# Kernel tuning notes

Measured on AMD Instinct MI355X. Metric: run time of the kernel, lower is better.

The kernel has to match this reference:

```python
import jax, jax.numpy as jnp
import numpy as np

N_NODES = 100000
N_EDGES = 1600000
N_FEAT = 4
HIDDEN = 128
EMBED = 128
N_GRAPHS = 512


def setup_inputs() -> dict:
    key = jax.random.key(0)
    ks = jax.random.split(key, 12)
    x = jax.random.normal(ks[0], (N_NODES, N_FEAT), dtype=jnp.float32)
    edge_index = jax.random.randint(ks[1], (2, N_EDGES), 0, N_NODES, dtype=jnp.int64)
    batch = jnp.sort(jax.random.randint(ks[2], (N_NODES,), 0, N_GRAPHS, dtype=jnp.int64))
    def glorot(k, fan_in, fan_out):
        s = jnp.sqrt(6.0 / (fan_in + fan_out))
        return jax.random.uniform(k, (fan_in, fan_out), jnp.float32, -s, s)
    return {
        "x": x,
        "edge_index": edge_index,
        "batch": batch,
        "W_d1": glorot(ks[3], N_FEAT, N_FEAT),
        "b_d1": jnp.zeros((N_FEAT,), jnp.float32),
        "W_g1": glorot(ks[4], N_FEAT, HIDDEN),
        "b_g1": jnp.zeros((HIDDEN,), jnp.float32),
        "W_g2": glorot(ks[5], HIDDEN, HIDDEN),
        "b_g2": jnp.zeros((HIDDEN,), jnp.float32),
        "W_g3": glorot(ks[6], HIDDEN, HIDDEN),
        "b_g3": jnp.zeros((HIDDEN,), jnp.float32),
        "W_d2": glorot(ks[7], HIDDEN, EMBED),
        "b_d2": jnp.zeros((EMBED,), jnp.float32),
    }


def _gcn(x, W, b, src, dst, norm, n_nodes):
    # GCNConv: out[dst] += norm_e * (x @ W)[src], plus bias
    h = x @ W                      # [N, Dout]
    msg = h[src] * norm[:, None]   # [E+N, Dout] (self-loops included)
    out = jax.ops.segment_sum(msg, dst, num_segments=n_nodes)
    return out + b


def reference(x, edge_index, batch, W_d1, b_d1, W_g1, b_g1, W_g2, b_g2, W_g3, b_g3, W_d2, b_d2):
    n = x.shape[0]
    # add self-loops (PyG GCNConv default add_self_loops=True)
    loop = jnp.arange(n, dtype=edge_index.dtype)
    src = jnp.concatenate([edge_index[0], loop])
    dst = jnp.concatenate([edge_index[1], loop])
    # symmetric degree normalization: deg computed over target (col)
    deg = jax.ops.segment_sum(jnp.ones_like(dst, dtype=x.dtype), dst, num_segments=n)
    dis = jnp.where(deg > 0, jax.lax.rsqrt(jnp.maximum(deg, 1.0)), 0.0)
    norm = dis[src] * dis[dst]     # [E+N]

    h = jax.nn.relu(x @ W_d1 + b_d1)
    h = jax.nn.relu(_gcn(h, W_g1, b_g1, src, dst, norm, n))
    h = jax.nn.relu(_gcn(h, W_g2, b_g2, src, dst, norm, n))
    h = jax.nn.relu(_gcn(h, W_g3, b_g3, src, dst, norm, n))

    # global_mean_pool over batch assignment
    sums = jax.ops.segment_sum(h, batch, num_segments=N_GRAPHS)
    cnts = jax.ops.segment_sum(jnp.ones((n,), h.dtype), batch, num_segments=N_GRAPHS)
    pooled = sums / jnp.maximum(cnts, 1.0)[:, None]
    # dropout p=0.3 is identity in eval mode
    return pooled @ W_d2 + b_d2
```

## Files before the change

kernel.cpp:

```cpp
#include <hip/hip_runtime.h>
#include <hip/hip_fp16.h>


#define BSHIFT 8
#define BSZ    256
#define MAXBKT 512
#define CPAD   32
#define CAPSH  13

typedef _Float16 half8 __attribute__((ext_vector_type(8)));
typedef float f32x4 __attribute__((ext_vector_type(4)));
typedef float f32x2 __attribute__((ext_vector_type(2)));

#define RFL __builtin_amdgcn_readfirstlane

__global__ __launch_bounds__(512) void k_prep(
        const float* __restrict__ x, const float* __restrict__ Wd1,
        const float* __restrict__ bd1, __half* __restrict__ h0,
        const float* __restrict__ W2, const float* __restrict__ W3,
        __half* __restrict__ WT2, __half* __restrict__ WT3,
        const int* __restrict__ batch, int* __restrict__ gs,
        const int* __restrict__ src, const int* __restrict__ dst,
        int* __restrict__ bktFill, int* __restrict__ staged,
        float* __restrict__ sums,
        int N, int NG, int E, int nbkt, int BINB, int L1B, int NB1) {
    __shared__ int hh[MAXBKT], base[MAXBKT], cur[MAXBKT];
    int bid = blockIdx.x;
    int t = threadIdx.x;
    if (bid < BINB) {
        for (int i = t; i < nbkt; i += 512) { hh[i] = 0; cur[i] = 0; }
        __syncthreads();
        int e0 = bid * 4096 + t;
#pragma unroll
        for (int k = 0; k < 8; k++) {
            int e = e0 + k * 512;
            if (e < E) atomicAdd(&hh[dst[e] >> BSHIFT], 1);
        }
        __syncthreads();
        for (int i = t; i < nbkt; i += 512)
            base[i] = hh[i] ? atomicAdd(&bktFill[(size_t)i * CPAD], hh[i]) : 0;
        __syncthreads();
#pragma unroll
        for (int k = 0; k < 8; k++) {
            int e = e0 + k * 512;
            if (e < E) {
                int d = dst[e], s = src[e];
                int b = d >> BSHIFT;
                int off = atomicAdd(&cur[b], 1);
                staged[((size_t)b << CAPSH) + base[b] + off] =
                    ((d & (BSZ - 1)) << 17) | s;
            }
        }
    } else if (bid < BINB + L1B) {
        int node = (bid - BINB) * 512 + t;
        if (node < N) {
            float4 xv = ((const float4*)x)[node];
            float h[4];
#pragma unroll
            for (int k = 0; k < 4; k++) {
                float v = xv.x * Wd1[k] + xv.y * Wd1[4 + k]
                        + xv.z * Wd1[8 + k] + xv.w * Wd1[12 + k] + bd1[k];
                h[k] = fmaxf(v, 0.f);
            }
            __half2 o01 = __floats2half2_rn(h[0], h[1]);
            __half2 o23 = __floats2half2_rn(h[2], h[3]);
            uint2 pk;
            pk.x = *(unsigned*)&o01; pk.y = *(unsigned*)&o23;
            *(uint2*)(h0 + (size_t)node * 4) = pk;
        }
    } else if (bid < BINB + L1B + 32) {
        int t2 = (bid - BINB - L1B) * 512 + t;
        int k = t2 >> 7, nn = t2 & 127;
        WT2[nn * 128 + k] = __float2half_rn(W2[t2]);
        WT3[nn * 128 + k] = __float2half_rn(W3[t2]);
    } else if (bid < BINB + L1B + 32 + NB1) {
        int i = (bid - BINB - L1B - 32) * 512 + t;
        if (i >= N) return;
        int b = batch[i];
        int prev = (i == 0) ? -1 : batch[i - 1];
        for (int g2 = prev + 1; g2 <= b; ++g2) gs[g2] = i;
        if (i == N - 1)
            for (int g2 = b + 1; g2 <= NG; ++g2) gs[g2] = N;
    } else {
        int idx = (bid - BINB - L1B - 32 - NB1) * 512 + t;
        if (idx < NG * 128) sums[idx] = 0.f;
    }
}

__global__ __launch_bounds__(1024) void k_fineB(
        const int* __restrict__ staged, const int* __restrict__ bktFill,
        int2* __restrict__ rpe, float* __restrict__ dis,
        int* __restrict__ col, const __half* __restrict__ h0,
        __half* __restrict__ h0s, int N) {
    __shared__ int sEnt[1 << CAPSH];
    __shared__ int cnt[BSZ];
    __shared__ int incl[BSZ];
    int b = blockIdx.x;
    int lo = b << CAPSH;
    int cntE = bktFill[(size_t)b * CPAD];
    int n0 = b << BSHIFT;
    int tid = threadIdx.x;
    if (tid < BSZ) cnt[tid] = 0;
    __syncthreads();
    for (int e = tid; e < cntE; e += 1024) {
        int v = staged[lo + e];
        sEnt[e] = v;
        atomicAdd(&cnt[v >> 17], 1);
    }
    __syncthreads();
    int v = 0;
    if (tid < BSZ) { v = cnt[tid]; incl[tid] = v; }
    for (int off = 1; off < BSZ; off <<= 1) {
        __syncthreads();
        int t = (tid < BSZ && tid >= off) ? incl[tid - off] : 0;
        __syncthreads();
        if (tid < BSZ) incl[tid] += t;
    }
    __syncthreads();
    int myofs = 0;
    if (tid < BSZ) {
        myofs = incl[tid] - v;
        int node = n0 + tid;
        if (node < N) {
            rpe[node] = make_int2(lo + myofs, lo + myofs + v);
            float dloc = rsqrtf((float)(v + 1));
            dis[node] = dloc;
            uint2 hv = *(const uint2*)(h0 + (size_t)node * 4);
            float2 a01 = __half22float2(*(__half2*)&hv.x);
            float2 a23 = __half22float2(*(__half2*)&hv.y);
            __half2 o01 = __floats2half2_rn(a01.x * dloc, a01.y * dloc);
            __half2 o23 = __floats2half2_rn(a23.x * dloc, a23.y * dloc);
            uint2 pk;
            pk.x = *(unsigned*)&o01; pk.y = *(unsigned*)&o23;
            *(uint2*)(h0s + (size_t)node * 4) = pk;
        }
    }
    __syncthreads();
    if (tid < BSZ) { incl[tid] = myofs; cnt[tid] = 0; }
    __syncthreads();
    for (int e = tid; e < cntE; e += 1024) {
        int ent = sEnt[e];
        int dl = ent >> 17;
        int pos = lo + incl[dl] + atomicAdd(&cnt[dl], 1);
        col[pos] = ent & 0x1FFFF;
    }
}

__device__ __forceinline__ void addv4(float a[4], uint2 v) {
    float2 x01 = __half22float2(*(__half2*)&v.x);
    float2 x23 = __half22float2(*(__half2*)&v.y);
    a[0] += x01.x; a[1] += x01.y; a[2] += x23.x; a[3] += x23.y;
}

__global__ __launch_bounds__(256) void k_agg4(
        const __half* __restrict__ h0s, const int2* __restrict__ rpe,
        const float* __restrict__ dis, const int* __restrict__ col,
        float4* __restrict__ agg4, int N) {
    int n = blockIdx.x * 256 + threadIdx.x;
    if (n >= N) return;
    int2 re = rpe[n];
    float di = dis[n];
    float a[4];
    {
        uint2 sv = *(const uint2*)(h0s + (size_t)n * 4);
        float2 s01 = __half22float2(*(__half2*)&sv.x);
        float2 s23 = __half22float2(*(__half2*)&sv.y);
        a[0] = s01.x; a[1] = s01.y; a[2] = s23.x; a[3] = s23.y;
    }
    int e = re.x, r1 = re.y;
    for (; e + 3 < r1; e += 4) {
        int c0 = col[e], c1 = col[e + 1], c2 = col[e + 2], c3 = col[e + 3];
        uint2 v0 = *(const uint2*)(h0s + (size_t)c0 * 4);
        uint2 v1 = *(const uint2*)(h0s + (size_t)c1 * 4);
        uint2 v2 = *(const uint2*)(h0s + (size_t)c2 * 4);
        uint2 v3 = *(const uint2*)(h0s + (size_t)c3 * 4);
        addv4(a, v0); addv4(a, v1); addv4(a, v2); addv4(a, v3);
    }
    for (; e < r1; ++e) {
        uint2 v0 = *(const uint2*)(h0s + (size_t)col[e] * 4);
        addv4(a, v0);
    }
    agg4[n] = make_float4(di * a[0], di * a[1], di * a[2], di * a[3]);
}

__device__ __forceinline__ uint2 pack_fp8x8(const float v[8]) {
    int a = 0, b = 0;
    a = __builtin_amdgcn_cvt_pk_fp8_f32(v[0], v[1], a, false);
    a = __builtin_amdgcn_cvt_pk_fp8_f32(v[2], v[3], a, true);
    b = __builtin_amdgcn_cvt_pk_fp8_f32(v[4], v[5], b, false);
    b = __builtin_amdgcn_cvt_pk_fp8_f32(v[6], v[7], b, true);
    return make_uint2((unsigned)a, (unsigned)b);
}

__device__ __forceinline__ void accf8(float acc[4], unsigned u) {
    f32x2 lo = __builtin_amdgcn_cvt_pk_f32_fp8(u, false);
    f32x2 hi = __builtin_amdgcn_cvt_pk_f32_fp8(u, true);
    acc[0] += lo[0]; acc[1] += lo[1]; acc[2] += hi[0]; acc[3] += hi[1];
}

__global__ __launch_bounds__(256) void k_mmL1(
        const float4* __restrict__ agg4, const float* __restrict__ Wg1,
        const float* __restrict__ b1, const __half* __restrict__ WT2,
        const float* __restrict__ dis, unsigned char* __restrict__ qout,
        int n) {
    __shared__ float sW[512];
    __shared__ float sB[128];
    __shared__ _Float16 sH[16 * 136];
    __shared__ _Float16 sO[16 * 136];
    __shared__ float sDis[16];
    int t = threadIdx.x;
    sW[t] = Wg1[t];
    sW[t + 256] = Wg1[t + 256];
    if (t < 128) sB[t] = b1[t];
    int node0 = blockIdx.x * 16;
    int row = t >> 4, seg = t & 15;
    if (t < 16) sDis[t] = (node0 + t < n) ? dis[node0 + t] : 0.f;
    int nodeR = node0 + row;
    float4 av = (nodeR < n) ? agg4[nodeR] : make_float4(0.f, 0.f, 0.f, 0.f);
    __syncthreads();
    half8 hv;
#pragma unroll
    for (int u = 0; u < 8; u++) {
        int j = seg * 8 + u;
        float vv = sB[j] + av.x * sW[j] + av.y * sW[128 + j]
                 + av.z * sW[256 + j] + av.w * sW[384 + j];
        hv[u] = (_Float16)fmaxf(vv, 0.f);
    }
    *(half8*)&sH[row * 136 + seg * 8] = hv;
    __syncthreads();
    int wave = t >> 6, lane = t & 63;
    int q = lane >> 4, c = lane & 15;
    int n0 = wave * 32;
    f32x4 acc0 = {0.f, 0.f, 0.f, 0.f}, acc1 = {0.f, 0.f, 0.f, 0.f};
#pragma unroll
    for (int ks = 0; ks < 4; ks++) {
        int k0 = ks * 32;
        half8 a  = *(half8*)&sH[c * 136 + k0 + q * 8];
        half8 b0 = *(const half8*)(WT2 + (size_t)(n0 + c) * 128 + k0 + q * 8);
        half8 b1v = *(const half8*)(WT2 + (size_t)(n0 + 16 + c) * 128 + k0 + q * 8);
        acc0 = __builtin_amdgcn_mfma_f32_16x16x32_f16(a, b0, acc0, 0, 0, 0);
        acc1 = __builtin_amdgcn_mfma_f32_16x16x32_f16(a, b1v, acc1, 0, 0, 0);
    }
#pragma unroll
    for (int r = 0; r < 4; r++) {
        int rr = q * 4 + r;
        sO[rr * 136 + n0 + c]      = (_Float16)(acc0[r] * sDis[rr]);
        sO[rr * 136 + n0 + 16 + c] = (_Float16)(acc1[r] * sDis[rr]);
    }
    __syncthreads();
    half8 ov = *(half8*)&sO[row * 136 + seg * 8];
    float vv[8];
#pragma unroll
    for (int u = 0; u < 8; u++) vv[u] = (float)ov[u];
    if (nodeR < n)
        *(uint2*)(qout + (size_t)nodeR * 128 + seg * 8) = pack_fp8x8(vv);
}

__device__ __forceinline__ void agg_chunk_f8(
        const unsigned char* __restrict__ g, int colv, int nloc,
        int hf, int sl, float acc[4]) {
    int npair = nloc >> 1;
    int p = 0;
    for (; p + 3 < npair; p += 4) {
        int i2 = p * 2 + hf;
        int s0 = __shfl(colv, i2);
        int s1 = __shfl(colv, i2 + 2);
        int s2 = __shfl(colv, i2 + 4);
        int s3 = __shfl(colv, i2 + 6);
        unsigned u0 = *(const unsigned*)(g + (size_t)s0 * 128 + sl * 4);
        unsigned u1 = *(const unsigned*)(g + (size_t)s1 * 128 + sl * 4);
        unsigned u2 = *(const unsigned*)(g + (size_t)s2 * 128 + sl * 4);
        unsigned u3 = *(const unsigned*)(g + (size_t)s3 * 128 + sl * 4);
        accf8(acc, u0); accf8(acc, u1); accf8(acc, u2); accf8(acc, u3);
    }
    for (; p < npair; ++p) {
        int s0 = __shfl(colv, p * 2 + hf);
        unsigned u0 = *(const unsigned*)(g + (size_t)s0 * 128 + sl * 4);
        accf8(acc, u0);
    }
    if (nloc & 1) {
        int s0 = __shfl(colv, nloc - 1);
        unsigned u0 = *(const unsigned*)(g + (size_t)s0 * 128 + sl * 4);
        if (!hf) accf8(acc, u0);
    }
}

__device__ __forceinline__ void agg_node_f8v(
        const unsigned char* __restrict__ g, const int* __restrict__ col,
        int r0, int r1, int node, int colv, int hf, int sl, int lane,
        float acc[4]) {
    acc[0] = acc[1] = acc[2] = acc[3] = 0.f;
    if (!hf) {
        unsigned su = *(const unsigned*)(g + (size_t)node * 128 + sl * 4);
        accf8(acc, su);
    }
    int deg = r1 - r0;
    int nloc = deg < 64 ? deg : 64;
    agg_chunk_f8(g, colv, nloc, hf, sl, acc);
    for (int base = r0 + 64; base < r1; base += 64) {
        int cv = col[base + lane];
        int nl = r1 - base; if (nl > 64) nl = 64;
        agg_chunk_f8(g, cv, nl, hf, sl, acc);
    }
#pragma unroll
    for (int k = 0; k < 4; k++) acc[k] += __shfl_xor(acc[k], 32);
}

__global__ __launch_bounds__(256) void k_aggmm(
        const unsigned char* __restrict__ qin, const int2* __restrict__ rpe,
        const int* __restrict__ col, const float* __restrict__ dis,
        const float* __restrict__ bias, const __half* __restrict__ WT,
        unsigned char* __restrict__ qout, int n) {
    __shared__ _Float16 sH[16 * 136];
    __shared__ _Float16 sO[16 * 136];
    __shared__ float sDis[16];
    int t = threadIdx.x;
    int wave = t >> 6, lane = t & 63;
    int hf = lane >> 5, sl = lane & 31;
    int node0 = blockIdx.x * 16;
    if (t < 16) sDis[t] = (node0 + t < n) ? dis[node0 + t] : 0.f;
    float4 bb = ((const float4*)bias)[sl];
    int nodeA = node0 + wave * 4;
    int nd0 = RFL(nodeA), nd1 = RFL(nodeA + 1);
    int nd2 = RFL(nodeA + 2), nd3 = RFL(nodeA + 3);
    int r00 = 0, r10 = 0, r01 = 0, r11 = 0;
    int r02 = 0, r12 = 0, r03 = 0, r13 = 0;
    if (nd0 < n) { int2 re = rpe[nd0]; r00 = RFL(re.x); r10 = RFL(re.y); }
    if (nd1 < n) { int2 re = rpe[nd1]; r01 = RFL(re.x); r11 = RFL(re.y); }
    if (nd2 < n) { int2 re = rpe[nd2]; r02 = RFL(re.x); r12 = RFL(re.y); }
    if (nd3 < n) { int2 re = rpe[nd3]; r03 = RFL(re.x); r13 = RFL(re.y); }
    int cv0 = col[r00 + lane];
    int cv1 = col[r01 + lane];
    int cv2 = col[r02 + lane];
    int cv3 = col[r03 + lane];
    float acc[4];
#define AGGMM_NODE(I, ND, R0, R1, CV)                                        \
    if (ND < n) {                                                            \
        agg_node_f8v(qin, col, R0, R1, ND, CV, hf, sl, lane, acc);           \
        if (hf == 0) {                                                       \
            float di = sDis[wave * 4 + I];                                   \
            __half2 o01 = __floats2half2_rn(                                 \
                fmaxf(fmaf(di, acc[0], bb.x), 0.f),                          \
                fmaxf(fmaf(di, acc[1], bb.y), 0.f));                         \
            __half2 o23 = __floats2half2_rn(                                 \
                fmaxf(fmaf(di, acc[2], bb.z), 0.f),                          \
                fmaxf(fmaf(di, acc[3], bb.w), 0.f));                         \
            uint2 pk;                                                        \
            pk.x = *(unsigned*)&o01; pk.y = *(unsigned*)&o23;                \
            *(uint2*)&sH[(wave * 4 + I) * 136 + sl * 4] = pk;                \
        }                                                                    \
    }
    __syncthreads();
    AGGMM_NODE(0, nd0, r00, r10, cv0)
    AGGMM_NODE(1, nd1, r01, r11, cv1)
    AGGMM_NODE(2, nd2, r02, r12, cv2)
    AGGMM_NODE(3, nd3, r03, r13, cv3)
#undef AGGMM_NODE
    __syncthreads();
    int q = lane >> 4, c = lane & 15;
    int n0 = wave * 32;
    f32x4 acc0 = {0.f, 0.f, 0.f, 0.f}, acc1 = {0.f, 0.f, 0.f, 0.f};
#pragma unroll
    for (int ks = 0; ks < 4; ks++) {
        int k0 = ks * 32;
        half8 a  = *(half8*)&sH[c * 136 + k0 + q * 8];
        half8 b0 = *(const half8*)(WT + (size_t)(n0 + c) * 128 + k0 + q * 8);
        half8 b1 = *(const half8*)(WT + (size_t)(n0 + 16 + c) * 128 + k0 + q * 8);
        acc0 = __builtin_amdgcn_mfma_f32_16x16x32_f16(a, b0, acc0, 0, 0, 0);
        acc1 = __builtin_amdgcn_mfma_f32_16x16x32_f16(a, b1, acc1, 0, 0, 0);
    }
#pragma unroll
    for (int r = 0; r < 4; r++) {
        int rr = q * 4 + r;
        sO[rr * 136 + n0 + c]      = (_Float16)(acc0[r] * sDis[rr]);
        sO[rr * 136 + n0 + 16 + c] = (_Float16)(acc1[r] * sDis[rr]);
    }
    __syncthreads();
    int lr2 = t >> 4, seg = t & 15;
    int rowN = node0 + lr2;
    half8 ov = *(half8*)&sO[lr2 * 136 + seg * 8];
    float vv[8];
#pragma unroll
    for (int u = 0; u < 8; u++) vv[u] = (float)ov[u];
    if (rowN < n)
        *(uint2*)(qout + (size_t)rowN * 128 + seg * 8) = pack_fp8x8(vv);
}

__global__ __launch_bounds__(256) void k_aggsum(
        const unsigned char* __restrict__ qin, const int2* __restrict__ rpe,
        const int* __restrict__ col, const float* __restrict__ dis,
        const float* __restrict__ bias, const int* __restrict__ batch,
        float* __restrict__ sums, int n) {
    __shared__ float ls[4][128];
    int t = threadIdx.x;
    int wave = t >> 6, lane = t & 63;
    int hf = lane >> 5, sl = lane & 31;
    int nodeBase = blockIdx.x * 16;
    if (nodeBase >= n) return;
    int lastNode = min(nodeBase + 15, n - 1);
    int b0 = RFL(batch[nodeBase]);
    bool uni = (RFL(batch[lastNode]) == b0);
    float4 bb = ((const float4*)bias)[sl];
    float sx[4] = {0.f, 0.f, 0.f, 0.f};
    int curb = b0;
    int nodeA = nodeBase + wave * 4;
    int nd0 = RFL(nodeA), nd1 = RFL(nodeA + 1);
    int nd2 = RFL(nodeA + 2), nd3 = RFL(nodeA + 3);
    int r00 = 0, r10 = 0, r01 = 0, r11 = 0;
    int r02 = 0, r12 = 0, r03 = 0, r13 = 0;
    if (nd0 < n) { int2 re = rpe[nd0]; r00 = RFL(re.x); r10 = RFL(re.y); }
    if (nd1 < n) { int2 re = rpe[nd1]; r01 = RFL(re.x); r11 = RFL(re.y); }
    if (nd2 < n) { int2 re = rpe[nd2]; r02 = RFL(re.x); r12 = RFL(re.y); }
    if (nd3 < n) { int2 re = rpe[nd3]; r03 = RFL(re.x); r13 = RFL(re.y); }
    int cv0 = col[r00 + lane];
    int cv1 = col[r01 + lane];
    int cv2 = col[r02 + lane];
    int cv3 = col[r03 + lane];
    float acc[4];
#define AGGSUM_NODE(ND, R0, R1, CV)                                          \
    if (ND < n) {                                                            \
        agg_node_f8v(qin, col, R0, R1, ND, CV, hf, sl, lane, acc);           \
        float di = dis[ND];                                                  \
        float o0 = fmaxf(fmaf(di, acc[0], bb.x), 0.f);                       \
        float o1 = fmaxf(fmaf(di, acc[1], bb.y), 0.f);                       \
        float o2 = fmaxf(fmaf(di, acc[2], bb.z), 0.f);                       \
        float o3 = fmaxf(fmaf(di, acc[3], bb.w), 0.f);                       \
        if (!uni) {                                                          \
            int b = RFL(batch[ND]);                                          \
            if (b != curb) {                                                 \
                if (hf == 0) {                                               \
                    atomicAdd(&sums[(size_t)curb * 128 + sl * 4 + 0], sx[0]);\
                    atomicAdd(&sums[(size_t)curb * 128 + sl * 4 + 1], sx[1]);\
                    atomicAdd(&sums[(size_t)curb * 128 + sl * 4 + 2], sx[2]);\
                    atomicAdd(&sums[(size_t)curb * 128 + sl * 4 + 3], sx[3]);\
                }                                                            \
                sx[0] = sx[1] = sx[2] = sx[3] = 0.f;                         \
                curb = b;                                                    \
            }                                                                \
        }                                                                    \
        sx[0] += o0; sx[1] += o1; sx[2] += o2; sx[3] += o3;                  \
    }
    AGGSUM_NODE(nd0, r00, r10, cv0)
    AGGSUM_NODE(nd1, r01, r11, cv1)
    AGGSUM_NODE(nd2, r02, r12, cv2)
    AGGSUM_NODE(nd3, r03, r13, cv3)
#undef AGGSUM_NODE
    if (uni) {
        if (hf == 0) {
            ls[wave][sl * 4 + 0] = sx[0];
            ls[wave][sl * 4 + 1] = sx[1];
            ls[wave][sl * 4 + 2] = sx[2];
            ls[wave][sl * 4 + 3] = sx[3];
        }
        __syncthreads();
        if (t < 128) {
            float v = ls[0][t] + ls[1][t] + ls[2][t] + ls[3][t];
            atomicAdd(&sums[(size_t)b0 * 128 + t], v);
        }
    } else {
        if (hf == 0) {
            atomicAdd(&sums[(size_t)curb * 128 + sl * 4 + 0], sx[0]);
            atomicAdd(&sums[(size_t)curb * 128 + sl * 4 + 1], sx[1]);
            atomicAdd(&sums[(size_t)curb * 128 + sl * 4 + 2], sx[2]);
            atomicAdd(&sums[(size_t)curb * 128 + sl * 4 + 3], sx[3]);
        }
    }
}

__global__ __launch_bounds__(128) void k_head(
        const float* __restrict__ sums, const int* __restrict__ gs,
        const float* __restrict__ Wd2, const float* __restrict__ bd2,
        float* __restrict__ out) {
    int gidx = blockIdx.x;
    int j = threadIdx.x;
    int c = gs[gidx + 1] - gs[gidx];
    float inv = 1.0f / (float)(c > 1 ? c : 1);
    __shared__ float sp[128];
    sp[j] = sums[(size_t)gidx * 128 + j] * inv;
    __syncthreads();
    float o = bd2[j];
#pragma unroll 8
    for (int k = 0; k < 128; k++) o = fmaf(sp[k], Wd2[k * 128 + j], o);
    out[gidx * 128 + j] = o;
}

extern "C" void kernel_launch(void* const* d_in, const int* in_sizes, int n_in,
                              void* d_out, int out_size, void* d_ws, size_t ws_size,
                              hipStream_t stream) {
    const float* x   = (const float*)d_in[0];
    const int*  ei   = (const int*)d_in[1];
    const int* batch = (const int*)d_in[2];
    const float* Wd1 = (const float*)d_in[3];
    const float* bd1 = (const float*)d_in[4];
    const float* Wg1 = (const float*)d_in[5];
    const float* bg1 = (const float*)d_in[6];
    const float* Wg2 = (const float*)d_in[7];
    const float* bg2 = (const float*)d_in[8];
    const float* Wg3 = (const float*)d_in[9];
    const float* bg3 = (const float*)d_in[10];
    const float* Wd2 = (const float*)d_in[11];
    const float* bd2 = (const float*)d_in[12];
    float* out = (float*)d_out;

    int N  = in_sizes[0] / 4;
    int E  = in_sizes[1] / 2;
    int NG = out_size / 128;
    const int* srcIdx = ei;
    const int* dstIdx = ei + E;
    int nbkt = (N + BSZ - 1) >> BSHIFT;

    char* p = (char*)d_ws;
    auto alloc = [&](size_t bytes) -> char* {
        char* r = p;
        p += (bytes + 255) & ~(size_t)255;
        return r;
    };
    int*    bktFill = (int*)alloc((size_t)nbkt * CPAD * 4);
    int*    staged  = (int*)alloc(((size_t)nbkt << CAPSH) * 4);
    int*    col     = (int*)alloc(((size_t)nbkt << CAPSH) * 4 + 256);
    int2*   rpe     = (int2*)alloc((size_t)N * 8);
    float*  dis     = (float*)alloc((size_t)N * 4);
    int*    gs      = (int*)alloc(((size_t)NG + 1) * 4);
    float*  sums    = (float*)alloc((size_t)NG * 128 * 4);
    __half* WT2     = (__half*)alloc(16384 * 2);
    __half* WT3     = (__half*)alloc(16384 * 2);
    unsigned char* qB = (unsigned char*)alloc((size_t)N * 128);
    unsigned char* qA = (unsigned char*)alloc((size_t)N * 128);
    __half* h0      = (__half*)alloc((size_t)N * 4 * 2);
    __half* h0s     = (__half*)alloc((size_t)N * 4 * 2);
    float4* agg4    = (float4*)alloc((size_t)N * 16);
    (void)ws_size; (void)n_in;

    int BINB = (E + 4095) / 4096;
    int L1B  = (N + 511) / 512;
    int NB1  = (N + 511) / 512;
    int ZB   = (NG * 128 + 511) / 512;
    int prepB = BINB + L1B + 32 + NB1 + ZB;
    int nb16 = (N + 15) / 16;

    hipMemsetAsync(bktFill, 0, (size_t)nbkt * CPAD * 4, stream);

    k_prep<<<prepB, 512, 0, stream>>>(x, Wd1, bd1, h0, Wg2, Wg3, WT2, WT3,
                                      batch, gs, srcIdx, dstIdx, bktFill,
                                      staged, sums, N, NG, E, nbkt,
                                      BINB, L1B, NB1);
    k_fineB<<<nbkt, 1024, 0, stream>>>(staged, bktFill, rpe, dis, col,
                                       h0, h0s, N);

    k_agg4<<<(N + 255) / 256, 256, 0, stream>>>(h0s, rpe, dis, col, agg4, N);
    k_mmL1<<<nb16, 256, 0, stream>>>(agg4, Wg1, bg1, WT2, dis, qB, N);
    k_aggmm<<<nb16, 256, 0, stream>>>(qB, rpe, col, dis, bg2, WT3, qA, N);
    k_aggsum<<<nb16, 256, 0, stream>>>(qA, rpe, col, dis, bg3, batch,
                                       sums, N);

    k_head<<<NG, 128, 0, stream>>>(sums, gs, Wd2, bd2, out);
}
```

Baseline: 265.3 us.

## Fuse layer-1 4-wide aggregation into L1 matmul kernel; unroll fp8 gather by 8

Merges the standalone per-node 4-feature aggregation kernel into the layer-1 transform/MFMA kernel. Each node's neighbor list is now gathered by 16 lanes and combined with xor shuffles, where before one thread walked the whole list. This removes a kernel launch and the agg4 global round trip, and spreads the gather across more threads. The fp8 gather loop used by the later layers also gains an 8-way unrolled stage, putting more independent loads in flight at some cost in registers.

```diff
diff --git a/kernel.cpp b/kernel.cpp
--- a/kernel.cpp
+++ b/kernel.cpp
@@ -152,37 +152,6 @@
     a[0] += x01.x; a[1] += x01.y; a[2] += x23.x; a[3] += x23.y;
 }
 
-__global__ __launch_bounds__(256) void k_agg4(
-        const __half* __restrict__ h0s, const int2* __restrict__ rpe,
-        const float* __restrict__ dis, const int* __restrict__ col,
-        float4* __restrict__ agg4, int N) {
-    int n = blockIdx.x * 256 + threadIdx.x;
-    if (n >= N) return;
-    int2 re = rpe[n];
-    float di = dis[n];
-    float a[4];
-    {
-        uint2 sv = *(const uint2*)(h0s + (size_t)n * 4);
-        float2 s01 = __half22float2(*(__half2*)&sv.x);
-        float2 s23 = __half22float2(*(__half2*)&sv.y);
-        a[0] = s01.x; a[1] = s01.y; a[2] = s23.x; a[3] = s23.y;
-    }
-    int e = re.x, r1 = re.y;
-    for (; e + 3 < r1; e += 4) {
-        int c0 = col[e], c1 = col[e + 1], c2 = col[e + 2], c3 = col[e + 3];
-        uint2 v0 = *(const uint2*)(h0s + (size_t)c0 * 4);
-        uint2 v1 = *(const uint2*)(h0s + (size_t)c1 * 4);
-        uint2 v2 = *(const uint2*)(h0s + (size_t)c2 * 4);
-        uint2 v3 = *(const uint2*)(h0s + (size_t)c3 * 4);
-        addv4(a, v0); addv4(a, v1); addv4(a, v2); addv4(a, v3);
-    }
-    for (; e < r1; ++e) {
-        uint2 v0 = *(const uint2*)(h0s + (size_t)col[e] * 4);
-        addv4(a, v0);
-    }
-    agg4[n] = make_float4(di * a[0], di * a[1], di * a[2], di * a[3]);
-}
-
 __device__ __forceinline__ uint2 pack_fp8x8(const float v[8]) {
     int a = 0, b = 0;
     a = __builtin_amdgcn_cvt_pk_fp8_f32(v[0], v[1], a, false);
@@ -198,54 +167,85 @@
     acc[0] += lo[0]; acc[1] += lo[1]; acc[2] += hi[0]; acc[3] += hi[1];
 }
 
-__global__ __launch_bounds__(256) void k_mmL1(
-        const float4* __restrict__ agg4, const float* __restrict__ Wg1,
-        const float* __restrict__ b1, const __half* __restrict__ WT2,
-        const float* __restrict__ dis, unsigned char* __restrict__ qout,
+__global__ __launch_bounds__(256) void k_aggL1(
+        const __half* __restrict__ h0s, const int2* __restrict__ rpe,
+        const float* __restrict__ dis, const int* __restrict__ col,
+        const float* __restrict__ Wg1, const float* __restrict__ b1,
+        const __half* __restrict__ WT2, unsigned char* __restrict__ qout,
         int n) {
     __shared__ float sW[512];
     __shared__ float sB[128];
+    __shared__ float sAgg[16][4];
+    __shared__ float sDis[16];
     __shared__ _Float16 sH[16 * 136];
     __shared__ _Float16 sO[16 * 136];
-    __shared__ float sDis[16];
     int t = threadIdx.x;
     sW[t] = Wg1[t];
     sW[t + 256] = Wg1[t + 256];
     if (t < 128) sB[t] = b1[t];
     int node0 = blockIdx.x * 16;
+    if (t < 16) sDis[t] = (node0 + t < n) ? dis[node0 + t] : 0.f;
+    int g = t >> 4, sub = t & 15;
+    int ng = node0 + g;
+    float a[4] = {0.f, 0.f, 0.f, 0.f};
+    if (ng < n) {
+        int2 re = rpe[ng];
+        int r0 = re.x, r1 = re.y;
+        for (int e = r0 + sub; e < r1; e += 16) {
+            uint2 vv = *(const uint2*)(h0s + (size_t)col[e] * 4);
+            addv4(a, vv);
+        }
+    }
+#pragma unroll
+    for (int k = 0; k < 4; k++) {
+        a[k] += __shfl_xor(a[k], 1);
+        a[k] += __shfl_xor(a[k], 2);
+        a[k] += __shfl_xor(a[k], 4);
+        a[k] += __shfl_xor(a[k], 8);
+    }
+    if (ng < n) {
+        uint2 sv = *(const uint2*)(h0s + (size_t)ng * 4);
+        float2 s01 = __half22float2(*(__half2*)&sv.x);
+        float2 s23 = __half22float2(*(__half2*)&sv.y);
+        a[0] += s01.x; a[1] += s01.y; a[2] += s23.x; a[3] += s23.y;
+        float di = dis[ng];
+        float av = (sub == 0) ? a[0] : (sub == 1) ? a[1]
+                 : (sub == 2) ? a[2] : a[3];
+        if (sub < 4) sAgg[g][sub] = av * di;
+    }
+    __syncthreads();
     int row = t >> 4, seg = t & 15;
-    if (t < 16) sDis[t] = (node0 + t < n) ? dis[node0 + t] : 0.f;
     int nodeR = node0 + row;
-    float4 av = (nodeR < n) ? agg4[nodeR] : make_float4(0.f, 0.f, 0.f, 0.f);
-    __syncthreads();
+    float4 av4 = make_float4(sAgg[row][0], sAgg[row][1],
+                             sAgg[row][2], sAgg[row][3]);
     half8 hv;
 #pragma unroll
     for (int u = 0; u < 8; u++) {
         int j = seg * 8 + u;
-        float vv = sB[j] + av.x * sW[j] + av.y * sW[128 + j]
-                 + av.z * sW[256 + j] + av.w * sW[384 + j];
+        float vv = sB[j] + av4.x * sW[j] + av4.y * sW[128 + j]
+                 + av4.z * sW[256 + j] + av4.w * sW[384 + j];
         hv[u] = (_Float16)fmaxf(vv, 0.f);
     }
     *(half8*)&sH[row * 136 + seg * 8] = hv;
     __syncthreads();
     int wave = t >> 6, lane = t & 63;
     int q = lane >> 4, c = lane & 15;
-    int n0 = wave * 32;
+    int n0c = wave * 32;
     f32x4 acc0 = {0.f, 0.f, 0.f, 0.f}, acc1 = {0.f, 0.f, 0.f, 0.f};
 #pragma unroll
     for (int ks = 0; ks < 4; ks++) {
         int k0 = ks * 32;
-        half8 a  = *(half8*)&sH[c * 136 + k0 + q * 8];
-        half8 b0 = *(const half8*)(WT2 + (size_t)(n0 + c) * 128 + k0 + q * 8);
-        half8 b1v = *(const half8*)(WT2 + (size_t)(n0 + 16 + c) * 128 + k0 + q * 8);
-        acc0 = __builtin_amdgcn_mfma_f32_16x16x32_f16(a, b0, acc0, 0, 0, 0);
-        acc1 = __builtin_amdgcn_mfma_f32_16x16x32_f16(a, b1v, acc1, 0, 0, 0);
+        half8 av  = *(half8*)&sH[c * 136 + k0 + q * 8];
+        half8 b0 = *(const half8*)(WT2 + (size_t)(n0c + c) * 128 + k0 + q * 8);
+        half8 b1v = *(const half8*)(WT2 + (size_t)(n0c + 16 + c) * 128 + k0 + q * 8);
+        acc0 = __builtin_amdgcn_mfma_f32_16x16x32_f16(av, b0, acc0, 0, 0, 0);
+        acc1 = __builtin_amdgcn_mfma_f32_16x16x32_f16(av, b1v, acc1, 0, 0, 0);
     }
 #pragma unroll
     for (int r = 0; r < 4; r++) {
         int rr = q * 4 + r;
-        sO[rr * 136 + n0 + c]      = (_Float16)(acc0[r] * sDis[rr]);
-        sO[rr * 136 + n0 + 16 + c] = (_Float16)(acc1[r] * sDis[rr]);
+        sO[rr * 136 + n0c + c]      = (_Float16)(acc0[r] * sDis[rr]);
+        sO[rr * 136 + n0c + 16 + c] = (_Float16)(acc1[r] * sDis[rr]);
     }
     __syncthreads();
     half8 ov = *(half8*)&sO[row * 136 + seg * 8];
@@ -261,6 +261,27 @@
         int hf, int sl, float acc[4]) {
     int npair = nloc >> 1;
     int p = 0;
+    for (; p + 7 < npair; p += 8) {
+        int i2 = p * 2 + hf;
+        int s0 = __shfl(colv, i2);
+        int s1 = __shfl(colv, i2 + 2);
+        int s2 = __shfl(colv, i2 + 4);
+        int s3 = __shfl(colv, i2 + 6);
+        int s4 = __shfl(colv, i2 + 8);
+        int s5 = __shfl(colv, i2 + 10);
+        int s6 = __shfl(colv, i2 + 12);
+        int s7 = __shfl(colv, i2 + 14);
+        unsigned u0 = *(const unsigned*)(g + (size_t)s0 * 128 + sl * 4);
+        unsigned u1 = *(const unsigned*)(g + (size_t)s1 * 128 + sl * 4);
+        unsigned u2 = *(const unsigned*)(g + (size_t)s2 * 128 + sl * 4);
+        unsigned u3 = *(const unsigned*)(g + (size_t)s3 * 128 + sl * 4);
+        unsigned u4 = *(const unsigned*)(g + (size_t)s4 * 128 + sl * 4);
+        unsigned u5 = *(const unsigned*)(g + (size_t)s5 * 128 + sl * 4);
+        unsigned u6 = *(const unsigned*)(g + (size_t)s6 * 128 + sl * 4);
+        unsigned u7 = *(const unsigned*)(g + (size_t)s7 * 128 + sl * 4);
+        accf8(acc, u0); accf8(acc, u1); accf8(acc, u2); accf8(acc, u3);
+        accf8(acc, u4); accf8(acc, u5); accf8(acc, u6); accf8(acc, u7);
+    }
     for (; p + 3 < npair; p += 4) {
         int i2 = p * 2 + hf;
         int s0 = __shfl(colv, i2);
@@ -528,7 +549,6 @@
     unsigned char* qA = (unsigned char*)alloc((size_t)N * 128);
     __half* h0      = (__half*)alloc((size_t)N * 4 * 2);
     __half* h0s     = (__half*)alloc((size_t)N * 4 * 2);
-    float4* agg4    = (float4*)alloc((size_t)N * 16);
     (void)ws_size; (void)n_in;
 
     int BINB = (E + 4095) / 4096;
@@ -547,8 +567,8 @@
     k_fineB<<<nbkt, 1024, 0, stream>>>(staged, bktFill, rpe, dis, col,
                                        h0, h0s, N);
 
-    k_agg4<<<(N + 255) / 256, 256, 0, stream>>>(h0s, rpe, dis, col, agg4, N);
-    k_mmL1<<<nb16, 256, 0, stream>>>(agg4, Wg1, bg1, WT2, dis, qB, N);
+    k_aggL1<<<nb16, 256, 0, stream>>>(h0s, rpe, dis, col, Wg1, bg1, WT2,
+                                      qB, N);
     k_aggmm<<<nb16, 256, 0, stream>>>(qB, rpe, col, dis, bg2, WT3, qA, N);
     k_aggsum<<<nb16, 256, 0, stream>>>(qA, rpe, col, dis, bg3, batch,
                                        sums, N);
```

After: 262.4 us. Within noise of the previous version (-1.1%).
